# Optimization experiments

Measured on AMD Instinct MI355X. Metric: run time of the kernel, lower is better.

Reference implementation:

```python
import jax, jax.numpy as jnp
import numpy as np

NS, L, H = 8, 2048, 1024
M, E, K = 4096, 8, 2
EPS = 1e-9

def setup_inputs() -> dict:
    key = jax.random.key(0)
    ks = jax.random.split(key, 5)
    s = 0.02
    return {
        "x": jax.random.normal(ks[0], (NS, L, H), jnp.float32),
        "Wr": jax.random.normal(ks[1], (H, E), jnp.float32) * s,
        "br": jnp.zeros((E,), jnp.float32),
        "W1": jax.random.normal(ks[2], (E, H, M), jnp.float32) * s,
        "b1": jnp.zeros((E, M), jnp.float32),
        "W2": jax.random.normal(ks[3], (E, M, H), jnp.float32) * s,
        "b2": jnp.zeros((E, H), jnp.float32),
    }

def reference(x, Wr, br, W1, b1, W2, b2):
    ns, seq, h = x.shape
    flat = x.reshape(-1, h)                      # (N, H); grouping only reshapes, math is per-token
    logits = flat @ Wr + br                      # (N, E)
    probs = jax.nn.softmax(logits, axis=-1)
    vals, idx = jax.lax.top_k(probs, K)          # (N, K)
    w = vals / (jnp.sum(vals, axis=-1, keepdims=True) + EPS)
    out_acc = jnp.zeros_like(flat)
    weight_acc = jnp.zeros((flat.shape[0],), flat.dtype)
    for e in range(E):                           # fixed small expert loop
        we = jnp.sum(w * (idx == e), axis=-1)    # (N,) combine weight for expert e
        hmid = jax.nn.gelu(flat @ W1[e] + b1[e], approximate=False)
        y = hmid @ W2[e] + b2[e]
        out_acc = out_acc + we[:, None] * y
        weight_acc = weight_acc + we
    out = out_acc / (weight_acc[:, None] + EPS)
    return out.reshape(ns, seq, h)
```

## Files before the change

### kernel.cpp

```cpp
#include <hip/hip_runtime.h>
#include <hip/hip_bf16.h>
#include <math.h>

#define NTOK 16384
#define HDIM 1024
#define MDIM 4096
#define NEXP 8
#define EPSV 1e-9f
#define RTOK 32

typedef unsigned short u16;
typedef __attribute__((ext_vector_type(4))) float f32x4;
typedef __attribute__((ext_vector_type(8))) __bf16 bf16x8;
typedef __attribute__((ext_vector_type(8))) unsigned short u16x8;
typedef __attribute__((ext_vector_type(4))) unsigned short u16x4;

#define ASYNC_COPY16(gptr, lptr) \
    __builtin_amdgcn_global_load_lds( \
        (const __attribute__((address_space(1))) void*)(gptr), \
        (__attribute__((address_space(3))) void*)(lptr), 16, 0, 0)

static __device__ __forceinline__ u16 f2bf(float f) {
    unsigned int u = __builtin_bit_cast(unsigned int, f);
    u += 0x7fff + ((u >> 16) & 1);
    return (u16)(u >> 16);
}

static __device__ __forceinline__ float gelu_f(float v) {
    float z2 = -1.5957691216f * v * (1.f + 0.044715f * v * v);
    return v / (1.f + __expf(z2));
}

__global__ __launch_bounds__(256) void router_kernel(
    const float* __restrict__ x, const float* __restrict__ Wr,
    const float* __restrict__ br,
    int* __restrict__ counts, int* __restrict__ ltok, float* __restrict__ lcf,
    u16* __restrict__ xb)
{
    __shared__ int   lcount[NEXP];
    __shared__ int   lbase[NEXP];
    __shared__ int   ltokL[NEXP][RTOK];
    __shared__ float lcfL[NEXP][RTOK];

    int t = threadIdx.x;
    if (t < NEXP) lcount[t] = 0;
    __syncthreads();

    int wave = t >> 6, lane = t & 63;

    for (int it = 0; it < RTOK / 4; ++it) {
        int tok = blockIdx.x * RTOK + it * 4 + wave;
        const float* xr = x + (size_t)tok * HDIM + lane * 16;

        f32x4 xv[4];
        #pragma unroll
        for (int q = 0; q < 4; q++) xv[q] = *reinterpret_cast<const f32x4*>(xr + q * 4);

        u16x8 ob0, ob1;
        #pragma unroll
        for (int j = 0; j < 4; j++) {
            ob0[j]     = f2bf(xv[0][j]);
            ob0[4 + j] = f2bf(xv[1][j]);
            ob1[j]     = f2bf(xv[2][j]);
            ob1[4 + j] = f2bf(xv[3][j]);
        }
        u16* xo = xb + (size_t)tok * HDIM + lane * 16;
        *reinterpret_cast<u16x8*>(xo)     = ob0;
        *reinterpret_cast<u16x8*>(xo + 8) = ob1;

        f32x4 acc0 = {0.f, 0.f, 0.f, 0.f};
        f32x4 acc1 = {0.f, 0.f, 0.f, 0.f};
        #pragma unroll
        for (int q = 0; q < 4; q++) {
            #pragma unroll
            for (int j = 0; j < 4; j++) {
                int h = lane * 16 + q * 4 + j;
                const float* wrow = Wr + (size_t)h * NEXP;
                f32x4 w0 = *reinterpret_cast<const f32x4*>(wrow);
                f32x4 w1 = *reinterpret_cast<const f32x4*>(wrow + 4);
                acc0 += xv[q][j] * w0;
                acc1 += xv[q][j] * w1;
            }
        }
        float a[NEXP];
        #pragma unroll
        for (int e = 0; e < 4; e++) { a[e] = acc0[e]; a[4 + e] = acc1[e]; }
        #pragma unroll
        for (int e = 0; e < NEXP; e++) {
            #pragma unroll
            for (int s = 1; s < 64; s <<= 1) a[e] += __shfl_xor(a[e], s, 64);
        }
        if (lane == 0) {
            float l[NEXP], m = -1e30f;
            #pragma unroll
            for (int e = 0; e < NEXP; e++) { l[e] = a[e] + br[e]; m = fmaxf(m, l[e]); }
            float p[NEXP], s = 0.f;
            #pragma unroll
            for (int e = 0; e < NEXP; e++) { p[e] = expf(l[e] - m); s += p[e]; }
            int i0 = 0; float v0 = p[0];
            #pragma unroll
            for (int e = 1; e < NEXP; e++) if (p[e] > v0) { v0 = p[e]; i0 = e; }
            int i1 = -1; float v1 = -1.f;
            #pragma unroll
            for (int e = 0; e < NEXP; e++) if (e != i0 && p[e] > v1) { v1 = p[e]; i1 = e; }
            v0 /= s; v1 /= s;
            float sw = v0 + v1;
            float w0 = v0 / (sw + EPSV), w1 = v1 / (sw + EPSV);
            float wa = w0 + w1;
            float c0 = w0 / (wa + EPSV), c1 = w1 / (wa + EPSV);
            int q0 = atomicAdd(&lcount[i0], 1);
            ltokL[i0][q0] = tok; lcfL[i0][q0] = c0;
            int q1 = atomicAdd(&lcount[i1], 1);
            ltokL[i1][q1] = tok; lcfL[i1][q1] = c1;
        }
    }
    __syncthreads();
    if (t < NEXP) lbase[t] = atomicAdd(&counts[t], lcount[t]);
    __syncthreads();
    #pragma unroll
    for (int e = 0; e < NEXP; e++) {
        int n = lcount[e], b = lbase[e];
        for (int j = t; j < n; j += 256) {
            ltok[e * NTOK + b + j] = ltokL[e][j];
            lcf[e * NTOK + b + j]  = lcfL[e][j];
        }
    }
}

__global__ void bases_kernel(const int* __restrict__ counts, int* __restrict__ bases)
{
    if (threadIdx.x == 0) {
        int acc = 0;
        #pragma unroll
        for (int e = 0; e < NEXP; e++) { bases[e] = acc; acc += counts[e]; }
    }
}

__global__ __launch_bounds__(256) void transpose_cvt_kernel(
    const float* __restrict__ in, u16* __restrict__ out, int R, int C)
{
    __shared__ float tile[32][33];
    const float* ine = in + (size_t)blockIdx.z * R * C;
    u16* oute = out + (size_t)blockIdx.z * R * C;
    int r0 = blockIdx.y * 32, c0 = blockIdx.x * 32;
    int t = threadIdx.x;
    int r = t >> 3, cq = t & 7;
    f32x4 v = *reinterpret_cast<const f32x4*>(ine + (size_t)(r0 + r) * C + c0 + cq * 4);
    #pragma unroll
    for (int j = 0; j < 4; j++) tile[r][cq * 4 + j] = v[j];
    __syncthreads();
    int c = t >> 3, rq = t & 7;
    u16x4 o;
    #pragma unroll
    for (int j = 0; j < 4; j++) o[j] = f2bf(tile[rq * 4 + j][c]);
    *reinterpret_cast<u16x4*>(oute + (size_t)(c0 + c) * R + r0 + rq * 4) = o;
}

template<int EPI>
__global__ __launch_bounds__(256) void gemm_kernel(
    const u16* __restrict__ A,
    const u16* __restrict__ BT_all,
    const float* __restrict__ bias_all,
    const int* __restrict__ counts,
    const int* __restrict__ bases,
    const int* __restrict__ ltok,
    const float* __restrict__ lcf,
    u16* __restrict__ hmid,
    float* __restrict__ out,
    int K, int P, int Astride, int eStart)
{
    int e = eStart + blockIdx.z;
    int nrows = counts[e];
    int row0 = blockIdx.y * 128;
    if (row0 >= nrows) return;
    int p0 = blockIdx.x * 128;
    int slotbase = bases[e];
    const u16*   BT   = BT_all + (size_t)e * P * K;
    const float* bias = bias_all + (size_t)e * P;
    const int*   lte  = ltok + (size_t)e * NTOK;
    const float* lcfe = lcf  + (size_t)e * NTOK;

    __shared__ u16 As[128][64];
    __shared__ u16 Bs[128][64];

    int t = threadIdx.x;
    int wv = t >> 6, lane = t & 63;
    int lrow8 = lane >> 3;
    int lcol8 = lane & 7;
    int schunk = lcol8 ^ lrow8;

    const u16* aptr[4];
    const u16* bptr[4];
    #pragma unroll
    for (int i = 0; i < 4; i++) {
        int pos  = row0 + wv * 32 + i * 8 + lrow8;
        int posc = min(pos, nrows - 1);
        int arow = (EPI == 0) ? lte[posc] : (slotbase + posc);
        aptr[i] = A + (size_t)arow * Astride + schunk * 8;
        int prow = p0 + wv * 32 + i * 8 + lrow8;
        bptr[i] = BT + (size_t)prow * K + schunk * 8;
    }

    int wr = (wv >> 1) * 64, wc = (wv & 1) * 64;
    int lr = lane & 15, lg = lane >> 4;
    int lr7 = lr & 7;

    f32x4 acc[4][4];
    #pragma unroll
    for (int m = 0; m < 4; m++)
        #pragma unroll
        for (int nn = 0; nn < 4; nn++) acc[m][nn] = (f32x4){0.f, 0.f, 0.f, 0.f};

    for (int k0 = 0; k0 < K; k0 += 64) {
        #pragma unroll
        for (int i = 0; i < 4; i++) {
            ASYNC_COPY16(aptr[i] + k0, &As[wv * 32 + i * 8][0]);
            ASYNC_COPY16(bptr[i] + k0, &Bs[wv * 32 + i * 8][0]);
        }
        __syncthreads();
        #pragma unroll
        for (int kk = 0; kk < 64; kk += 32) {
            bf16x8 af[4], bfr[4];
            #pragma unroll
            for (int m = 0; m < 4; m++)
                af[m] = *reinterpret_cast<const bf16x8*>(
                    &As[wr + m * 16 + lr][((((kk >> 3) + lg) ^ lr7)) * 8]);
            #pragma unroll
            for (int nn = 0; nn < 4; nn++)
                bfr[nn] = *reinterpret_cast<const bf16x8*>(
                    &Bs[wc + nn * 16 + lr][((((kk >> 3) + lg) ^ lr7)) * 8]);
            #pragma unroll
            for (int m = 0; m < 4; m++)
                #pragma unroll
                for (int nn = 0; nn < 4; nn++)
                    acc[m][nn] = __builtin_amdgcn_mfma_f32_16x16x32_bf16(
                        af[m], bfr[nn], acc[m][nn], 0, 0, 0);
        }
        __syncthreads();
    }

    if (EPI == 0) {
        #pragma unroll
        for (int m = 0; m < 4; m++) {
            #pragma unroll
            for (int r = 0; r < 4; r++) {
                int pos = row0 + wr + m * 16 + lg * 4 + r;
                if (pos < nrows) {
                    size_t ho = (size_t)(slotbase + pos) * MDIM;
                    #pragma unroll
                    for (int nn = 0; nn < 4; nn++) {
                        int col = p0 + wc + nn * 16 + lr;
                        float v = acc[m][nn][r] + bias[col];
                        hmid[ho + col] = f2bf(gelu_f(v));
                    }
                }
            }
        }
    } else {
        #pragma unroll
        for (int m = 0; m < 4; m++) {
            #pragma unroll
            for (int r = 0; r < 4; r++) {
                int pos = row0 + wr + m * 16 + lg * 4 + r;
                if (pos < nrows) {
                    int tokr = lte[pos];
                    float cf = lcfe[pos];
                    float* orow = out + (size_t)tokr * HDIM;
                    #pragma unroll
                    for (int nn = 0; nn < 4; nn++) {
                        int col = p0 + wc + nn * 16 + lr;
                        float v = (acc[m][nn][r] + bias[col]) * cf;
                        atomicAdd(orow + col, v);
                    }
                }
            }
        }
    }
}

extern "C" void kernel_launch(void* const* d_in, const int* in_sizes, int n_in,
                              void* d_out, int out_size, void* d_ws, size_t ws_size,
                              hipStream_t stream)
{
    const float* x  = (const float*)d_in[0];
    const float* Wr = (const float*)d_in[1];
    const float* br = (const float*)d_in[2];
    const float* W1 = (const float*)d_in[3];
    const float* b1 = (const float*)d_in[4];
    const float* W2 = (const float*)d_in[5];
    const float* b2 = (const float*)d_in[6];
    float* out = (float*)d_out;

    char* ws = (char*)d_ws;
    size_t off = 0;
    auto alloc = [&](size_t bytes) {
        void* p = ws + off;
        off = (off + bytes + 255) & ~(size_t)255;
        return p;
    };
    int*   counts = (int*)  alloc(NEXP * 4);
    int*   bases  = (int*)  alloc(NEXP * 4);
    int*   ltok   = (int*)  alloc((size_t)NEXP * NTOK * 4);
    float* lcf    = (float*)alloc((size_t)NEXP * NTOK * 4);
    u16*   xb     = (u16*)  alloc((size_t)NTOK * HDIM * 2);
    u16*   w1t    = (u16*)  alloc((size_t)NEXP * MDIM * HDIM * 2);
    u16*   w2t    = (u16*)  alloc((size_t)NEXP * HDIM * MDIM * 2);
    size_t fixed_end = off;
    bool grouped = (ws_size >= fixed_end + (size_t)2 * NTOK * MDIM * 2);
    u16* hmid = (u16*)alloc((grouped ? (size_t)2 * NTOK : (size_t)NTOK) * MDIM * 2);

    hipMemsetAsync(counts, 0, NEXP * 4, stream);
    hipMemsetAsync(d_out, 0, (size_t)out_size * sizeof(float), stream);

    transpose_cvt_kernel<<<dim3(MDIM / 32, HDIM / 32, NEXP), 256, 0, stream>>>(W1, w1t, HDIM, MDIM);
    transpose_cvt_kernel<<<dim3(HDIM / 32, MDIM / 32, NEXP), 256, 0, stream>>>(W2, w2t, MDIM, HDIM);
    router_kernel<<<NTOK / RTOK, 256, 0, stream>>>(x, Wr, br, counts, ltok, lcf, xb);

    if (grouped) {
        bases_kernel<<<1, 64, 0, stream>>>(counts, bases);
        gemm_kernel<0><<<dim3(MDIM / 128, NTOK / 128, NEXP), 256, 0, stream>>>(
            xb, w1t, b1, counts, bases, ltok, lcf, hmid, nullptr,
            HDIM, MDIM, HDIM, 0);
        gemm_kernel<1><<<dim3(HDIM / 128, NTOK / 128, NEXP), 256, 0, stream>>>(
            hmid, w2t, b2, counts, bases, ltok, lcf, nullptr, out,
            MDIM, HDIM, MDIM, 0);
    } else {
        hipMemsetAsync(bases, 0, NEXP * 4, stream);
        for (int e = 0; e < NEXP; e++) {
            gemm_kernel<0><<<dim3(MDIM / 128, NTOK / 128, 1), 256, 0, stream>>>(
                xb, w1t, b1, counts, bases, ltok, lcf, hmid, nullptr,
                HDIM, MDIM, HDIM, e);
            gemm_kernel<1><<<dim3(HDIM / 128, NTOK / 128, 1), 256, 0, stream>>>(
                hmid, w2t, b2, counts, bases, ltok, lcf, nullptr, out,
                MDIM, HDIM, MDIM, e);
        }
    }
}
```

Before: 994.9 us.

## Double-buffer GEMM LDS tiles and remap workgroups for XCD locality

Shared-memory A/B tiles are double-buffered so the async global-to-LDS copy of the next K step is issued before the MFMA work on the current one, with one barrier per iteration. Workgroup IDs are also remapped so consecutive logical tiles land on the same XCD, which is meant to improve L2 reuse of weight and activation tiles across the 8 chiplets. In exchange LDS use doubles to 64KB per block, which can lower occupancy. There is a possible race because the prefetch into the other buffer relies on the async load completing by the next barrier without an explicit vmcnt wait.

Result: slower. 1.185 ms (+19.1%).

```diff
diff --git a/kernel.cpp b/kernel.cpp
--- a/kernel.cpp
+++ b/kernel.cpp
@@ -156,7 +156,7 @@
     *reinterpret_cast<u16x4*>(oute + (size_t)(c0 + c) * R + r0 + rq * 4) = o;
 }
 
-template<int EPI>
+template<int EPI, int GX, int GY>
 __global__ __launch_bounds__(256) void gemm_kernel(
     const u16* __restrict__ A,
     const u16* __restrict__ BT_all,
@@ -169,19 +169,30 @@
     float* __restrict__ out,
     int K, int P, int Astride, int eStart)
 {
-    int e = eStart + blockIdx.z;
+    int gz = gridDim.z;
+    int nwg = GX * GY * gz;
+    int orig = blockIdx.x + GX * (blockIdx.y + GY * blockIdx.z);
+    int q = nwg >> 3, r = nwg & 7;
+    int xcd = orig & 7, sub = orig >> 3;
+    int wgid = (xcd < r ? xcd * (q + 1) : r * (q + 1) + (xcd - r) * q) + sub;
+    int bx = wgid & (GX - 1);
+    int rem = wgid / GX;
+    int by = rem & (GY - 1);
+    int bz = rem / GY;
+
+    int e = eStart + bz;
     int nrows = counts[e];
-    int row0 = blockIdx.y * 128;
+    int row0 = by * 128;
     if (row0 >= nrows) return;
-    int p0 = blockIdx.x * 128;
+    int p0 = bx * 128;
     int slotbase = bases[e];
     const u16*   BT   = BT_all + (size_t)e * P * K;
     const float* bias = bias_all + (size_t)e * P;
     const int*   lte  = ltok + (size_t)e * NTOK;
     const float* lcfe = lcf  + (size_t)e * NTOK;
 
-    __shared__ u16 As[128][64];
-    __shared__ u16 Bs[128][64];
+    __shared__ u16 As[2][128][64];
+    __shared__ u16 Bs[2][128][64];
 
     int t = threadIdx.x;
     int wv = t >> 6, lane = t & 63;
@@ -211,24 +222,31 @@
         #pragma unroll
         for (int nn = 0; nn < 4; nn++) acc[m][nn] = (f32x4){0.f, 0.f, 0.f, 0.f};
 
-    for (int k0 = 0; k0 < K; k0 += 64) {
+    auto stage = [&](int buf, int k0) {
         #pragma unroll
         for (int i = 0; i < 4; i++) {
-            ASYNC_COPY16(aptr[i] + k0, &As[wv * 32 + i * 8][0]);
-            ASYNC_COPY16(bptr[i] + k0, &Bs[wv * 32 + i * 8][0]);
-        }
-        __syncthreads();
+            ASYNC_COPY16(aptr[i] + k0, &As[buf][wv * 32 + i * 8][0]);
+            ASYNC_COPY16(bptr[i] + k0, &Bs[buf][wv * 32 + i * 8][0]);
+        }
+    };
+
+    stage(0, 0);
+    __syncthreads();
+    int nk = K >> 6;
+    int cur = 0;
+    for (int ks = 0; ks < nk; ks++) {
+        if (ks + 1 < nk) stage(cur ^ 1, (ks + 1) << 6);
         #pragma unroll
         for (int kk = 0; kk < 64; kk += 32) {
             bf16x8 af[4], bfr[4];
             #pragma unroll
             for (int m = 0; m < 4; m++)
                 af[m] = *reinterpret_cast<const bf16x8*>(
-                    &As[wr + m * 16 + lr][((((kk >> 3) + lg) ^ lr7)) * 8]);
+                    &As[cur][wr + m * 16 + lr][((((kk >> 3) + lg) ^ lr7)) * 8]);
             #pragma unroll
             for (int nn = 0; nn < 4; nn++)
                 bfr[nn] = *reinterpret_cast<const bf16x8*>(
-                    &Bs[wc + nn * 16 + lr][((((kk >> 3) + lg) ^ lr7)) * 8]);
+                    &Bs[cur][wc + nn * 16 + lr][((((kk >> 3) + lg) ^ lr7)) * 8]);
             #pragma unroll
             for (int m = 0; m < 4; m++)
                 #pragma unroll
@@ -237,20 +255,21 @@
                         af[m], bfr[nn], acc[m][nn], 0, 0, 0);
         }
         __syncthreads();
+        cur ^= 1;
     }
 
     if (EPI == 0) {
         #pragma unroll
         for (int m = 0; m < 4; m++) {
             #pragma unroll
-            for (int r = 0; r < 4; r++) {
-                int pos = row0 + wr + m * 16 + lg * 4 + r;
+            for (int r2 = 0; r2 < 4; r2++) {
+                int pos = row0 + wr + m * 16 + lg * 4 + r2;
                 if (pos < nrows) {
                     size_t ho = (size_t)(slotbase + pos) * MDIM;
                     #pragma unroll
                     for (int nn = 0; nn < 4; nn++) {
                         int col = p0 + wc + nn * 16 + lr;
-                        float v = acc[m][nn][r] + bias[col];
+                        float v = acc[m][nn][r2] + bias[col];
                         hmid[ho + col] = f2bf(gelu_f(v));
                     }
                 }
@@ -260,8 +279,8 @@
         #pragma unroll
         for (int m = 0; m < 4; m++) {
             #pragma unroll
-            for (int r = 0; r < 4; r++) {
-                int pos = row0 + wr + m * 16 + lg * 4 + r;
+            for (int r2 = 0; r2 < 4; r2++) {
+                int pos = row0 + wr + m * 16 + lg * 4 + r2;
                 if (pos < nrows) {
                     int tokr = lte[pos];
                     float cf = lcfe[pos];
@@ -269,7 +288,7 @@
                     #pragma unroll
                     for (int nn = 0; nn < 4; nn++) {
                         int col = p0 + wc + nn * 16 + lr;
-                        float v = (acc[m][nn][r] + bias[col]) * cf;
+                        float v = (acc[m][nn][r2] + bias[col]) * cf;
                         atomicAdd(orow + col, v);
                     }
                 }
@@ -318,19 +337,23 @@
 
     if (grouped) {
         bases_kernel<<<1, 64, 0, stream>>>(counts, bases);
-        gemm_kernel<0><<<dim3(MDIM / 128, NTOK / 128, NEXP), 256, 0, stream>>>(
+        gemm_kernel<0, MDIM / 128, NTOK / 128>
+            <<<dim3(MDIM / 128, NTOK / 128, NEXP), 256, 0, stream>>>(
             xb, w1t, b1, counts, bases, ltok, lcf, hmid, nullptr,
             HDIM, MDIM, HDIM, 0);
-        gemm_kernel<1><<<dim3(HDIM / 128, NTOK / 128, NEXP), 256, 0, stream>>>(
+        gemm_kernel<1, HDIM / 128, NTOK / 128>
+            <<<dim3(HDIM / 128, NTOK / 128, NEXP), 256, 0, stream>>>(
             hmid, w2t, b2, counts, bases, ltok, lcf, nullptr, out,
             MDIM, HDIM, MDIM, 0);
     } else {
         hipMemsetAsync(bases, 0, NEXP * 4, stream);
         for (int e = 0; e < NEXP; e++) {
-            gemm_kernel<0><<<dim3(MDIM / 128, NTOK / 128, 1), 256, 0, stream>>>(
+            gemm_kernel<0, MDIM / 128, NTOK / 128>
+                <<<dim3(MDIM / 128, NTOK / 128, 1), 256, 0, stream>>>(
                 xb, w1t, b1, counts, bases, ltok, lcf, hmid, nullptr,
                 HDIM, MDIM, HDIM, e);
-            gemm_kernel<1><<<dim3(HDIM / 128, NTOK / 128, 1), 256, 0, stream>>>(
+            gemm_kernel<1, HDIM / 128, NTOK / 128>
+                <<<dim3(HDIM / 128, NTOK / 128, 1), 256, 0, stream>>>(
                 hmid, w2t, b2, counts, bases, ltok, lcf, nullptr, out,
                 MDIM, HDIM, MDIM, e);
         }
```
